# Performance work log

Hardware: AMD Instinct MI355X
Metric: run time of the kernel (lower is better)

## Reference

```python
import jax, jax.numpy as jnp
import numpy as np

D_MODEL = 512
N_HEADS = 8
D_HEAD = D_MODEL // N_HEADS
EPS = 1e-5


def layer_norm(x, g, b):
    mu = jnp.mean(x, axis=-1, keepdims=True)
    var = jnp.mean(jnp.square(x - mu), axis=-1, keepdims=True)
    return (x - mu) * jax.lax.rsqrt(var + EPS) * g + b


def setup_inputs() -> dict:
    key = jax.random.key(0)
    ks = jax.random.split(key, 8)
    B, L, D = 2, 4096, D_MODEL
    x = jax.random.normal(ks[0], (B, L, D), dtype=jnp.float32)
    # monotonically increasing event timestamps (hours)
    timestamps = jnp.sort(jax.random.uniform(ks[1], (B, L), dtype=jnp.float32) * 1000.0, axis=-1)
    mask = jnp.ones((B, L), dtype=jnp.float32)
    s = 0.02
    return {
        "x": x,
        "timestamps": timestamps,
        "mask": mask,
        "ln1_g": jnp.ones((D,), jnp.float32),
        "ln1_b": jnp.zeros((D,), jnp.float32),
        "w_qkv": jax.random.normal(ks[2], (3 * D, D), jnp.float32) * s,
        "w_out": jax.random.normal(ks[3], (D, D), jnp.float32) * s,
        "decay_rate": jnp.ones((N_HEADS,), jnp.float32) * 0.01,
        "ln2_g": jnp.ones((D,), jnp.float32),
        "ln2_b": jnp.zeros((D,), jnp.float32),
        "w_ff1": jax.random.normal(ks[4], (4 * D, D), jnp.float32) * s,
        "w_ff2": jax.random.normal(ks[5], (D, 4 * D), jnp.float32) * s,
    }


def reference(x, timestamps, mask, ln1_g, ln1_b, w_qkv, w_out, decay_rate, ln2_g, ln2_b, w_ff1, w_ff2):
    B, L, D = x.shape
    H, dh = N_HEADS, D_HEAD
    scale = dh ** (-0.5)

    xn = layer_norm(x, ln1_g, ln1_b)
    qkv = (xn @ w_qkv.T).reshape(B, L, 3, H, dh).transpose(2, 0, 3, 1, 4)  # [3,B,H,L,dh]
    q, k, v = qkv[0], qkv[1], qkv[2]

    attn = jnp.einsum("bhid,bhjd->bhij", q, k) * scale  # [B,H,L,L]

    # temporal-decay bias
    t_diff = jnp.abs(timestamps[:, None, :, None] - timestamps[:, None, None, :]) / 24.0  # [B,1,L,L]
    decay = jax.nn.softplus(decay_rate)[None, :, None, None]  # [1,H,1,1]
    attn = attn - decay * t_diff

    # causal mask
    causal = jnp.triu(jnp.ones((L, L), dtype=bool), k=1)
    attn = jnp.where(causal[None, None], -jnp.inf, attn)

    # padding mask over keys
    pad = (mask == 0)[:, None, None, :]  # [B,1,1,L]
    attn = jnp.where(pad, -jnp.inf, attn)

    attn = jax.nn.softmax(attn, axis=-1)
    out = jnp.einsum("bhij,bhjd->bhid", attn, v).transpose(0, 2, 1, 3).reshape(B, L, D)

    x = x + out @ w_out.T
    h = layer_norm(x, ln2_g, ln2_b)
    x = x + jax.nn.silu(h @ w_ff1.T) @ w_ff2.T
    return x
```

## Files before the change

### kernel.cpp

```cpp
#include <hip/hip_runtime.h>
#include <hip/hip_bf16.h>
#include <cmath>


#define L_SEQ 4096
#define D_MODEL 512
#define N_HEADS 8
#define D_HEAD 64
#define QKV_LD 1536

typedef __attribute__((ext_vector_type(8))) short bf16x8;
typedef __attribute__((ext_vector_type(4))) float f32x4;
typedef __attribute__((ext_vector_type(4))) unsigned u32x4;

__device__ __forceinline__ __hip_bfloat16 f2bf(float v) { return __float2bfloat16(v); }

__device__ __forceinline__ float exp2_raw(float x) {
  float r;
  asm("v_exp_f32 %0, %1" : "=v"(r) : "v"(x));
  return r;
}

__device__ __forceinline__ void gl_lds16(const __hip_bfloat16* g, __hip_bfloat16* l) {
  __builtin_amdgcn_global_load_lds((__attribute__((address_space(1))) void*)g,
                                   (__attribute__((address_space(3))) void*)l, 16, 0, 0);
}

__global__ __launch_bounds__(256) void cvt4b_kernel(const float* __restrict__ s0, __hip_bfloat16* __restrict__ d0,
                                                    const float* __restrict__ s1, __hip_bfloat16* __restrict__ d1,
                                                    const float* __restrict__ s2, __hip_bfloat16* __restrict__ d2,
                                                    const float* __restrict__ s3, __hip_bfloat16* __restrict__ d3,
                                                    const float* __restrict__ ts,
                                                    const float* __restrict__ mask,
                                                    const float* __restrict__ decay_rate,
                                                    float* __restrict__ biasH) {
  const int i = blockIdx.x * 256 + threadIdx.x;
  if (i < 786432) {
    const float* s;
    __hip_bfloat16* d;
    int off;
    if (i < 196608) { s = s0; d = d0; off = i; }
    else if (i < 262144) { s = s1; d = d1; off = i - 196608; }
    else if (i < 524288) { s = s2; d = d2; off = i - 262144; }
    else { s = s3; d = d3; off = i - 524288; }
    const float4 v = ((const float4*)s)[off];
    d[4 * off + 0] = f2bf(v.x);
    d[4 * off + 1] = f2bf(v.y);
    d[4 * off + 2] = f2bf(v.z);
    d[4 * off + 3] = f2bf(v.w);
  } else {
    const int idx = i - 786432;
    const int col = idx & 4095;
    const int h = (idx >> 12) & 7;
    const int b = idx >> 15;
    const float LOG2E = 1.4426950408889634f;
    const float dfac = log1pf(expf(decay_rate[h])) * (1.0f / 24.0f) * LOG2E;
    const float m = mask[b * 4096 + col];
    biasH[idx] = dfac * ts[b * 4096 + col] + (m != 0.f ? 0.f : -1e30f);
  }
}

__global__ __launch_bounds__(256) void ln_kernel(const float* __restrict__ x,
                                                 const float* __restrict__ g,
                                                 const float* __restrict__ b,
                                                 __hip_bfloat16* __restrict__ out) {
  const int row = blockIdx.x;
  const int t = threadIdx.x;
  const float* xr = x + (size_t)row * D_MODEL;
  float v0 = xr[t];
  float v1 = xr[t + 256];
  float s = v0 + v1;
  float qq = v0 * v0 + v1 * v1;
  for (int off = 32; off > 0; off >>= 1) {
    s += __shfl_xor(s, off);
    qq += __shfl_xor(qq, off);
  }
  __shared__ float red[8];
  const int wid = t >> 6;
  if ((t & 63) == 0) { red[wid] = s; red[4 + wid] = qq; }
  __syncthreads();
  s = red[0] + red[1] + red[2] + red[3];
  qq = red[4] + red[5] + red[6] + red[7];
  const float mu = s * (1.0f / 512.0f);
  const float var = fmaxf(qq * (1.0f / 512.0f) - mu * mu, 0.0f);
  const float rstd = rsqrtf(var + 1e-5f);
  __hip_bfloat16* orow = out + (size_t)row * D_MODEL;
  orow[t] = f2bf((v0 - mu) * rstd * g[t] + b[t]);
  orow[t + 256] = f2bf((v1 - mu) * rstd * g[t + 256] + b[t + 256]);
}

__global__ __launch_bounds__(256) void vtrans_kernel(const __hip_bfloat16* __restrict__ qkv,
                                                     __hip_bfloat16* __restrict__ vt) {
  const int gid = blockIdx.x * 256 + threadIdx.x;
  const int l = gid & 4095;
  const int bg = gid >> 12;
  const int b = bg >> 6, g = bg & 63;
  const int h = g >> 3, dg = (g & 7) * 8;
  const __hip_bfloat16* src = qkv + (size_t)(b * L_SEQ + l) * QKV_LD + 1024 + h * 64 + dg;
  bf16x8 v = *(const bf16x8*)src;
  const int kin = l & 63;
  const int sl = (kin & 0x23) | ((kin & 0x10) >> 2) | ((kin & 0x0c) << 1);
  const size_t dbase = (size_t)((b * 8 + h) * 64 + dg) * L_SEQ + (l & ~63) + sl;
  for (int j = 0; j < 8; j++)
    vt[dbase + (size_t)j * L_SEQ] = ((const __hip_bfloat16*)&v)[j];
}

template <int EPI>
__global__ __launch_bounds__(256) void gemm_kernel(const __hip_bfloat16* __restrict__ A,
                                                   const __hip_bfloat16* __restrict__ B,
                                                   int M, int N, int K,
                                                   const float* __restrict__ aux,
                                                   void* __restrict__ C) {
  __shared__ __align__(16) __hip_bfloat16 As[2][128 * 32];
  __shared__ __align__(16) __hip_bfloat16 Bs[2][128 * 32];
  const int tid = threadIdx.x;
  const int lane = tid & 63, w = tid >> 6;
  const int m0 = blockIdx.y * 128, n0 = blockIdx.x * 128;
  const int wm = (w >> 1) * 64, wn = (w & 1) * 64;
  const int r = lane & 15, q = lane >> 4;

  f32x4 acc[4][4];
  const f32x4 zz = {0.f, 0.f, 0.f, 0.f};
  for (int i = 0; i < 4; i++)
    for (int j = 0; j < 4; j++) acc[i][j] = zz;

  const int c0 = tid, c1 = 256 + tid;
  const int row0 = c0 >> 2, kb0 = (c0 & 3) * 8;
  const int row1 = c1 >> 2, kb1 = (c1 & 3) * 8;

#define GEMM_STAGE(k0, buf)                                                     \
  do {                                                                          \
    gl_lds16(A + (size_t)(m0 + row0) * K + ((k0) + kb0), &As[buf][c0 * 8]);     \
    gl_lds16(B + (size_t)(n0 + row0) * K + ((k0) + kb0), &Bs[buf][c0 * 8]);     \
    gl_lds16(A + (size_t)(m0 + row1) * K + ((k0) + kb1), &As[buf][c1 * 8]);     \
    gl_lds16(B + (size_t)(n0 + row1) * K + ((k0) + kb1), &Bs[buf][c1 * 8]);     \
  } while (0)

  GEMM_STAGE(0, 0);
  const int niter = K >> 5;
  for (int it = 0; it < niter; it++) {
    const int cur = it & 1;
    if (it + 1 < niter) {
      GEMM_STAGE((it + 1) << 5, cur ^ 1);
      asm volatile("s_waitcnt vmcnt(4)" ::: "memory");
    } else {
      asm volatile("s_waitcnt vmcnt(0)" ::: "memory");
    }
    __builtin_amdgcn_s_barrier();
    bf16x8 af[4], bfr[4];
    for (int mi = 0; mi < 4; mi++)
      af[mi] = *(const bf16x8*)(&As[cur][(wm + mi * 16 + r) * 32 + q * 8]);
    for (int ni = 0; ni < 4; ni++)
      bfr[ni] = *(const bf16x8*)(&Bs[cur][(wn + ni * 16 + r) * 32 + q * 8]);
    for (int mi = 0; mi < 4; mi++)
      for (int ni = 0; ni < 4; ni++)
        acc[mi][ni] = __builtin_amdgcn_mfma_f32_16x16x32_bf16(af[mi], bfr[ni], acc[mi][ni], 0, 0, 0);
    __builtin_amdgcn_s_barrier();
  }
#undef GEMM_STAGE

  for (int mi = 0; mi < 4; mi++)
    for (int ni = 0; ni < 4; ni++)
      for (int j = 0; j < 4; j++) {
        const int gm = m0 + wm + mi * 16 + q * 4 + j;
        const int gn = n0 + wn + ni * 16 + r;
        float v = acc[mi][ni][j];
        const size_t idx = (size_t)gm * N + gn;
        if (EPI == 0) {
          ((__hip_bfloat16*)C)[idx] = f2bf(v);
        } else {
          v = v / (1.0f + expf(-v));
          ((__hip_bfloat16*)C)[idx] = f2bf(v);
        }
      }
}

__global__ __launch_bounds__(256) void gemm_res64_kernel(const __hip_bfloat16* __restrict__ A,
                                                         const __hip_bfloat16* __restrict__ B,
                                                         int M, int N, int K,
                                                         const float* __restrict__ aux,
                                                         float* __restrict__ C) {
  __shared__ __align__(16) __hip_bfloat16 As[2][64 * 32];
  __shared__ __align__(16) __hip_bfloat16 Bs[2][128 * 32];
  const int tid = threadIdx.x;
  const int lane = tid & 63, w = tid >> 6;
  const int m0 = blockIdx.y * 64, n0 = blockIdx.x * 128;
  const int wm = (w >> 1) * 32, wn = (w & 1) * 64;
  const int r = lane & 15, q = lane >> 4;

  f32x4 acc[2][4];
  const f32x4 zz = {0.f, 0.f, 0.f, 0.f};
  for (int i = 0; i < 2; i++)
    for (int j = 0; j < 4; j++) acc[i][j] = zz;

  const int rowA = tid >> 2, kbA = (tid & 3) * 8;
  const int c0 = tid, c1 = 256 + tid;
  const int rowB0 = c0 >> 2, kb0 = (c0 & 3) * 8;
  const int rowB1 = c1 >> 2, kb1 = (c1 & 3) * 8;

#define GEMM_STAGE64(k0, buf)                                                    \
  do {                                                                           \
    gl_lds16(A + (size_t)(m0 + rowA) * K + ((k0) + kbA), &As[buf][tid * 8]);     \
    gl_lds16(B + (size_t)(n0 + rowB0) * K + ((k0) + kb0), &Bs[buf][c0 * 8]);     \
    gl_lds16(B + (size_t)(n0 + rowB1) * K + ((k0) + kb1), &Bs[buf][c1 * 8]);     \
  } while (0)

  GEMM_STAGE64(0, 0);
  const int niter = K >> 5;
  for (int it = 0; it < niter; it++) {
    const int cur = it & 1;
    if (it + 1 < niter) {
      GEMM_STAGE64((it + 1) << 5, cur ^ 1);
      asm volatile("s_waitcnt vmcnt(3)" ::: "memory");
    } else {
      asm volatile("s_waitcnt vmcnt(0)" ::: "memory");
    }
    __builtin_amdgcn_s_barrier();
    bf16x8 af[2], bfr[4];
    for (int mi = 0; mi < 2; mi++)
      af[mi] = *(const bf16x8*)(&As[cur][(wm + mi * 16 + r) * 32 + q * 8]);
    for (int ni = 0; ni < 4; ni++)
      bfr[ni] = *(const bf16x8*)(&Bs[cur][(wn + ni * 16 + r) * 32 + q * 8]);
    for (int mi = 0; mi < 2; mi++)
      for (int ni = 0; ni < 4; ni++)
        acc[mi][ni] = __builtin_amdgcn_mfma_f32_16x16x32_bf16(af[mi], bfr[ni], acc[mi][ni], 0, 0, 0);
    __builtin_amdgcn_s_barrier();
  }
#undef GEMM_STAGE64

  for (int mi = 0; mi < 2; mi++)
    for (int ni = 0; ni < 4; ni++)
      for (int j = 0; j < 4; j++) {
        const int gm = m0 + wm + mi * 16 + q * 4 + j;
        const int gn = n0 + wn + ni * 16 + r;
        const size_t idx = (size_t)gm * N + gn;
        C[idx] = acc[mi][ni][j] + aux[idx];
      }
}

__device__ __forceinline__ void stage_kv128_w2(int w, int lane, int key0,
                                               const __hip_bfloat16* __restrict__ Kg,
                                               const __hip_bfloat16* __restrict__ Vg,
                                               __hip_bfloat16* Ks, __hip_bfloat16* Vs) {
  const int krow_in = lane >> 3;
  const int kcs = (lane & 7) ^ krow_in;
  const int vrow_in = lane >> 4;
  const int vch = lane & 15;
#pragma unroll
  for (int ii = 0; ii < 8; ii++) {
    const int i = w * 8 + ii;
    const int krow = i * 8 + krow_in;
    gl_lds16(Kg + (size_t)(key0 + krow) * QKV_LD + kcs * 8, Ks + i * 512 + lane * 8);
    const int vrow = i * 4 + vrow_in;
    const int vcs = vch ^ (vrow & 7);
    gl_lds16(Vg + (size_t)vrow * L_SEQ + key0 + vcs * 8, Vs + i * 512 + lane * 8);
  }
}

template <bool CAUSAL>
__device__ __forceinline__ void attn_tile128d(int key0, int lw0a, int r, int q,
                                              const __hip_bfloat16* Ks,
                                              const __hip_bfloat16* Vs,
                                              const float* biasLds, float scale2,
                                              const bf16x8& qfa0, const bf16x8& qfa1,
                                              const bf16x8& qfb0, const bf16x8& qfb1,
                                              const bf16x8& onesf,
                                              f32x4* oa, f32x4* ob, f32x4& lsa, f32x4& lsb) {
  const int r7 = r & 7;
  const f32x4 zz = {0.f, 0.f, 0.f, 0.f};
  f32x4 bias4[8];
#pragma unroll
  for (int hc = 0; hc < 8; hc++)
    bias4[hc] = *(const f32x4*)(biasLds + key0 + hc * 16 + q * 4);
  f32x4 sa[8], sb[8];
  __builtin_amdgcn_s_setprio(1);
#pragma unroll
  for (int hc = 0; hc < 8; hc++) {
    const __hip_bfloat16* kr = Ks + (hc * 16 + r) * 64;
    bf16x8 k0 = *(const bf16x8*)(kr + ((q ^ r7) * 8));
    bf16x8 k1 = *(const bf16x8*)(kr + (((q + 4) ^ r7) * 8));
    f32x4 a = __builtin_amdgcn_mfma_f32_16x16x32_bf16(k0, qfa0, zz, 0, 0, 0);
    a = __builtin_amdgcn_mfma_f32_16x16x32_bf16(k1, qfa1, a, 0, 0, 0);
    sa[hc] = a;
    f32x4 bb = __builtin_amdgcn_mfma_f32_16x16x32_bf16(k0, qfb0, zz, 0, 0, 0);
    bb = __builtin_amdgcn_mfma_f32_16x16x32_bf16(k1, qfb1, bb, 0, 0, 0);
    sb[hc] = bb;
  }
  __builtin_amdgcn_s_setprio(0);
  float pa_[8][4], pb_[8][4];
#pragma unroll
  for (int hc = 0; hc < 8; hc++)
#pragma unroll
    for (int j = 0; j < 4; j++) {
      const int key = key0 + hc * 16 + q * 4 + j;
      float pva = exp2_raw(fmaf(sa[hc][j], scale2, bias4[hc][j]));
      float pvb = exp2_raw(fmaf(sb[hc][j], scale2, bias4[hc][j]));
      if (CAUSAL) {
        pva = (key <= lw0a + r) ? pva : 0.f;
        pvb = (key <= lw0a + 16 + r) ? pvb : 0.f;
      }
      pa_[hc][j] = pva;
      pb_[hc][j] = pvb;
    }
  bf16x8 paa[4], pab[4];
#pragma unroll
  for (int kc = 0; kc < 4; kc++) {
    u32x4 pw;
    unsigned w0, w1, w2, w3;
    asm("v_cvt_pk_bf16_f32 %0, %1, %2" : "=v"(w0) : "v"(pa_[2 * kc][0]), "v"(pa_[2 * kc][1]));
    asm("v_cvt_pk_bf16_f32 %0, %1, %2" : "=v"(w1) : "v"(pa_[2 * kc][2]), "v"(pa_[2 * kc][3]));
    asm("v_cvt_pk_bf16_f32 %0, %1, %2" : "=v"(w2) : "v"(pa_[2 * kc + 1][0]), "v"(pa_[2 * kc + 1][1]));
    asm("v_cvt_pk_bf16_f32 %0, %1, %2" : "=v"(w3) : "v"(pa_[2 * kc + 1][2]), "v"(pa_[2 * kc + 1][3]));
    pw[0] = w0; pw[1] = w1; pw[2] = w2; pw[3] = w3;
    paa[kc] = *(bf16x8*)&pw;
    asm("v_cvt_pk_bf16_f32 %0, %1, %2" : "=v"(w0) : "v"(pb_[2 * kc][0]), "v"(pb_[2 * kc][1]));
    asm("v_cvt_pk_bf16_f32 %0, %1, %2" : "=v"(w1) : "v"(pb_[2 * kc][2]), "v"(pb_[2 * kc][3]));
    asm("v_cvt_pk_bf16_f32 %0, %1, %2" : "=v"(w2) : "v"(pb_[2 * kc + 1][0]), "v"(pb_[2 * kc + 1][1]));
    asm("v_cvt_pk_bf16_f32 %0, %1, %2" : "=v"(w3) : "v"(pb_[2 * kc + 1][2]), "v"(pb_[2 * kc + 1][3]));
    pw[0] = w0; pw[1] = w1; pw[2] = w2; pw[3] = w3;
    pab[kc] = *(bf16x8*)&pw;
  }
  __builtin_amdgcn_s_setprio(1);
#pragma unroll
  for (int kc = 0; kc < 4; kc++) {
#pragma unroll
    for (int c = 0; c < 4; c++) {
      const __hip_bfloat16* vr = Vs + (c * 16 + r) * 128 + (((kc * 4 + q) ^ r7) * 8);
      bf16x8 vf = *(const bf16x8*)vr;
      oa[c] = __builtin_amdgcn_mfma_f32_16x16x32_bf16(paa[kc], vf, oa[c], 0, 0, 0);
      ob[c] = __builtin_amdgcn_mfma_f32_16x16x32_bf16(pab[kc], vf, ob[c], 0, 0, 0);
    }
    lsa = __builtin_amdgcn_mfma_f32_16x16x32_bf16(paa[kc], onesf, lsa, 0, 0, 0);
    lsb = __builtin_amdgcn_mfma_f32_16x16x32_bf16(pab[kc], onesf, lsb, 0, 0, 0);
  }
  __builtin_amdgcn_s_setprio(0);
}

__global__ __launch_bounds__(128, 1) void attn_kernel(const __hip_bfloat16* __restrict__ qkv,
                                                      const __hip_bfloat16* __restrict__ vt,
                                                      const float* __restrict__ biasH,
                                                      __hip_bfloat16* __restrict__ out) {
  const int blk = blockIdx.x;
  const int bh = blk & 15;
  const int j = blk >> 4;
  const int b = bh >> 3, h = bh & 7;
  const int tid = threadIdx.x, lane = tid & 63, w = tid >> 6;
  const int r = lane & 15, q = lane >> 4;

  const int qi1 = j, qi2 = 63 - j;
  const int nt1 = (qi1 >> 1) + 1, nt2 = (qi2 >> 1) + 1;
  const int lwa1 = qi1 * 64 + w * 32;
  const int lwa2 = qi2 * 64 + w * 32;

  __shared__ __align__(16) __hip_bfloat16 Ksm[2][128 * 64];
  __shared__ __align__(16) __hip_bfloat16 Vsm[2][64 * 128];
  __shared__ __align__(16) float biasLds[4096];

  const float LOG2E = 1.4426950408889634f;
  const float scale2 = 0.125f * LOG2E;

  const __hip_bfloat16* Kg = qkv + (size_t)b * L_SEQ * QKV_LD + 512 + h * 64;
  const __hip_bfloat16* Vg = vt + (size_t)bh * 64 * L_SEQ;
  const float* biasHp = biasH + (size_t)bh * L_SEQ;

  stage_kv128_w2(w, lane, 0, Kg, Vg, Ksm[0], Vsm[0]);
#pragma unroll
  for (int ii = 0; ii < 8; ii++) {
    const int fo = (w * 8 + ii) * 256;
    gl_lds16((const __hip_bfloat16*)(biasHp + fo + lane * 4),
             (__hip_bfloat16*)(biasLds + fo + lane * 4));
  }

  bf16x8 qfa0, qfa1, qfb0, qfb1;
  {
    const __hip_bfloat16* qa = qkv + (size_t)(b * L_SEQ + lwa1 + r) * QKV_LD + h * 64 + q * 8;
    qfa0 = *(const bf16x8*)qa;
    qfa1 = *(const bf16x8*)(qa + 32);
    const __hip_bfloat16* qb = qa + (size_t)16 * QKV_LD;
    qfb0 = *(const bf16x8*)qb;
    qfb1 = *(const bf16x8*)(qb + 32);
  }

  const f32x4 zz = {0.f, 0.f, 0.f, 0.f};
  f32x4 oa[4], ob[4];
  for (int c = 0; c < 4; c++) { oa[c] = zz; ob[c] = zz; }
  f32x4 lsa = zz, lsb = zz;

  bf16x8 onesf;
  for (int i = 0; i < 8; i++) ((short*)&onesf)[i] = (short)0x3F80;

  for (int t = 0; t < nt1; t++) {
    const int cur = t & 1;
    const int nk = (t + 1 < nt1) ? (t + 1) : 0;
    stage_kv128_w2(w, lane, nk << 7, Kg, Vg, Ksm[cur ^ 1], Vsm[cur ^ 1]);
    asm volatile("s_waitcnt vmcnt(16)" ::: "memory");
    __builtin_amdgcn_s_barrier();
    if (t == nt1 - 1)
      attn_tile128d<true>(t << 7, lwa1, r, q, Ksm[cur], Vsm[cur], biasLds, scale2,
                          qfa0, qfa1, qfb0, qfb1, onesf, oa, ob, lsa, lsb);
    else
      attn_tile128d<false>(t << 7, lwa1, r, q, Ksm[cur], Vsm[cur], biasLds, scale2,
                           qfa0, qfa1, qfb0, qfb1, onesf, oa, ob, lsa, lsb);
    __builtin_amdgcn_s_barrier();
  }

  {
    float ija[4], ijb[4];
    for (int jj = 0; jj < 4; jj++) { ija[jj] = 1.0f / lsa[jj]; ijb[jj] = 1.0f / lsb[jj]; }
    for (int c = 0; c < 4; c++)
      for (int jj = 0; jj < 4; jj++) {
        const int ra = lwa1 + q * 4 + jj;
        out[(size_t)(b * L_SEQ + ra) * D_MODEL + h * 64 + c * 16 + r] = f2bf(oa[c][jj] * ija[jj]);
        out[(size_t)(b * L_SEQ + ra + 16) * D_MODEL + h * 64 + c * 16 + r] = f2bf(ob[c][jj] * ijb[jj]);
      }
    for (int c = 0; c < 4; c++) { oa[c] = zz; ob[c] = zz; }
    lsa = zz; lsb = zz;
    const __hip_bfloat16* qa = qkv + (size_t)(b * L_SEQ + lwa2 + r) * QKV_LD + h * 64 + q * 8;
    qfa0 = *(const bf16x8*)qa;
    qfa1 = *(const bf16x8*)(qa + 32);
    const __hip_bfloat16* qb = qa + (size_t)16 * QKV_LD;
    qfb0 = *(const bf16x8*)qb;
    qfb1 = *(const bf16x8*)(qb + 32);
  }

  for (int t = 0; t < nt2; t++) {
    const int cur = (nt1 + t) & 1;
    if (t + 1 < nt2) {
      stage_kv128_w2(w, lane, (t + 1) << 7, Kg, Vg, Ksm[cur ^ 1], Vsm[cur ^ 1]);
      asm volatile("s_waitcnt vmcnt(16)" ::: "memory");
    } else {
      asm volatile("s_waitcnt vmcnt(0)" ::: "memory");
    }
    __builtin_amdgcn_s_barrier();
    if (t == nt2 - 1)
      attn_tile128d<true>(t << 7, lwa2, r, q, Ksm[cur], Vsm[cur], biasLds, scale2,
                          qfa0, qfa1, qfb0, qfb1, onesf, oa, ob, lsa, lsb);
    else
      attn_tile128d<false>(t << 7, lwa2, r, q, Ksm[cur], Vsm[cur], biasLds, scale2,
                           qfa0, qfa1, qfb0, qfb1, onesf, oa, ob, lsa, lsb);
    __builtin_amdgcn_s_barrier();
  }

  {
    float ija[4], ijb[4];
    for (int jj = 0; jj < 4; jj++) { ija[jj] = 1.0f / lsa[jj]; ijb[jj] = 1.0f / lsb[jj]; }
    for (int c = 0; c < 4; c++)
      for (int jj = 0; jj < 4; jj++) {
        const int ra = lwa2 + q * 4 + jj;
        out[(size_t)(b * L_SEQ + ra) * D_MODEL + h * 64 + c * 16 + r] = f2bf(oa[c][jj] * ija[jj]);
        out[(size_t)(b * L_SEQ + ra + 16) * D_MODEL + h * 64 + c * 16 + r] = f2bf(ob[c][jj] * ijb[jj]);
      }
  }
}

extern "C" void kernel_launch(void* const* d_in, const int* in_sizes, int n_in,
                              void* d_out, int out_size, void* d_ws, size_t ws_size,
                              hipStream_t stream) {
  const float* x = (const float*)d_in[0];
  const float* ts = (const float*)d_in[1];
  const float* mask = (const float*)d_in[2];
  const float* ln1_g = (const float*)d_in[3];
  const float* ln1_b = (const float*)d_in[4];
  const float* w_qkv = (const float*)d_in[5];
  const float* w_out = (const float*)d_in[6];
  const float* decay = (const float*)d_in[7];
  const float* ln2_g = (const float*)d_in[8];
  const float* ln2_b = (const float*)d_in[9];
  const float* w_ff1 = (const float*)d_in[10];
  const float* w_ff2 = (const float*)d_in[11];

  char* ws = (char*)d_ws;
  __hip_bfloat16* wqkv_b = (__hip_bfloat16*)(ws + 0);
  __hip_bfloat16* wout_b = (__hip_bfloat16*)(ws + 1572864);
  __hip_bfloat16* wff1_b = (__hip_bfloat16*)(ws + 2097152);
  __hip_bfloat16* wff2_b = (__hip_bfloat16*)(ws + 4194304);
  __hip_bfloat16* xn = (__hip_bfloat16*)(ws + 6291456);
  __hip_bfloat16* vt = (__hip_bfloat16*)(ws + 6291456);
  __hip_bfloat16* qkv = (__hip_bfloat16*)(ws + 14680064);
  __hip_bfloat16* attnout = (__hip_bfloat16*)(ws + 39845888);
  __hip_bfloat16* h = attnout;
  __hip_bfloat16* ff1out = (__hip_bfloat16*)(ws + 6291456);
  float* x2 = (float*)(ws + 48234496);
  float* biasH = (float*)(ws + 48234496);
  float* out = (float*)d_out;

  const int M = 2 * L_SEQ;

  cvt4b_kernel<<<dim3(3328), dim3(256), 0, stream>>>(w_qkv, wqkv_b, w_out, wout_b,
                                                     w_ff1, wff1_b, w_ff2, wff2_b,
                                                     ts, mask, decay, biasH);

  ln_kernel<<<dim3(M), dim3(256), 0, stream>>>(x, ln1_g, ln1_b, xn);
  gemm_kernel<0><<<dim3(12, 64), dim3(256), 0, stream>>>(xn, wqkv_b, M, 1536, 512, nullptr, qkv);
  vtrans_kernel<<<dim3(2048), dim3(256), 0, stream>>>(qkv, vt);
  attn_kernel<<<dim3(512), dim3(128), 0, stream>>>(qkv, vt, biasH, attnout);
  gemm_res64_kernel<<<dim3(4, 128), dim3(256), 0, stream>>>(attnout, wout_b, M, 512, 512, x, x2);
  ln_kernel<<<dim3(M), dim3(256), 0, stream>>>(x2, ln2_g, ln2_b, h);
  gemm_kernel<2><<<dim3(16, 64), dim3(256), 0, stream>>>(h, wff1_b, M, 2048, 512, nullptr, ff1out);
  gemm_res64_kernel<<<dim3(4, 128), dim3(256), 0, stream>>>(ff1out, wff2_b, M, 512, 2048, x2, out);
}
```

Before: 295.0 us.

## Process paired causal query tiles concurrently with four waves sharing KV stages

The attention kernel goes from 2 waves that handle the short and long causal query tiles one after the other to 4 waves: two handle the short tile and two the long tile at the same time. The K/V tiles staged in LDS are shared by both groups, so each key block is loaded once per block instead of once per query tile. The KV loading work is spread over 4 waves and the waitcnt thresholds are adjusted to match. In exchange, the short-tile waves sit idle at barriers once their tile is finished, and the larger block may lower occupancy.

New measurement: 283.0 us. 4.1% less time.

```diff
diff --git a/kernel.cpp b/kernel.cpp
--- a/kernel.cpp
+++ b/kernel.cpp
@@ -238,7 +238,7 @@
       }
 }
 
-__device__ __forceinline__ void stage_kv128_w2(int w, int lane, int key0,
+__device__ __forceinline__ void stage_kv128_w4(int w, int lane, int key0,
                                                const __hip_bfloat16* __restrict__ Kg,
                                                const __hip_bfloat16* __restrict__ Vg,
                                                __hip_bfloat16* Ks, __hip_bfloat16* Vs) {
@@ -247,8 +247,8 @@
   const int vrow_in = lane >> 4;
   const int vch = lane & 15;
 #pragma unroll
-  for (int ii = 0; ii < 8; ii++) {
-    const int i = w * 8 + ii;
+  for (int ii = 0; ii < 4; ii++) {
+    const int i = w * 4 + ii;
     const int krow = i * 8 + krow_in;
     gl_lds16(Kg + (size_t)(key0 + krow) * QKV_LD + kcs * 8, Ks + i * 512 + lane * 8);
     const int vrow = i * 4 + vrow_in;
@@ -336,21 +336,19 @@
   __builtin_amdgcn_s_setprio(0);
 }
 
-__global__ __launch_bounds__(128, 1) void attn_kernel(const __hip_bfloat16* __restrict__ qkv,
+__global__ __launch_bounds__(256, 2) void attn_kernel(const __hip_bfloat16* __restrict__ qkv,
                                                       const __hip_bfloat16* __restrict__ vt,
                                                       const float* __restrict__ biasH,
                                                       __hip_bfloat16* __restrict__ out) {
   const int blk = blockIdx.x;
   const int bh = blk & 15;
-  const int j = blk >> 4;
+  const int pr = blk >> 4;
   const int b = bh >> 3, h = bh & 7;
   const int tid = threadIdx.x, lane = tid & 63, w = tid >> 6;
+  const int grp = w >> 1, wsub = w & 1;
+  const int qi = grp ? (63 - pr) : pr;
+  const int lw0a = qi * 64 + wsub * 32;
   const int r = lane & 15, q = lane >> 4;
-
-  const int qi1 = j, qi2 = 63 - j;
-  const int nt1 = (qi1 >> 1) + 1, nt2 = (qi2 >> 1) + 1;
-  const int lwa1 = qi1 * 64 + w * 32;
-  const int lwa2 = qi2 * 64 + w * 32;
 
   __shared__ __align__(16) __hip_bfloat16 Ksm[2][128 * 64];
   __shared__ __align__(16) __hip_bfloat16 Vsm[2][64 * 128];
@@ -363,17 +361,17 @@
   const __hip_bfloat16* Vg = vt + (size_t)bh * 64 * L_SEQ;
   const float* biasHp = biasH + (size_t)bh * L_SEQ;
 
-  stage_kv128_w2(w, lane, 0, Kg, Vg, Ksm[0], Vsm[0]);
-#pragma unroll
-  for (int ii = 0; ii < 8; ii++) {
-    const int fo = (w * 8 + ii) * 256;
+  stage_kv128_w4(w, lane, 0, Kg, Vg, Ksm[0], Vsm[0]);
+#pragma unroll
+  for (int ii = 0; ii < 4; ii++) {
+    const int fo = (w * 4 + ii) * 256;
     gl_lds16((const __hip_bfloat16*)(biasHp + fo + lane * 4),
              (__hip_bfloat16*)(biasLds + fo + lane * 4));
   }
 
   bf16x8 qfa0, qfa1, qfb0, qfb1;
   {
-    const __hip_bfloat16* qa = qkv + (size_t)(b * L_SEQ + lwa1 + r) * QKV_LD + h * 64 + q * 8;
+    const __hip_bfloat16* qa = qkv + (size_t)(b * L_SEQ + lw0a + r) * QKV_LD + h * 64 + q * 8;
     qfa0 = *(const bf16x8*)qa;
     qfa1 = *(const bf16x8*)(qa + 32);
     const __hip_bfloat16* qb = qa + (size_t)16 * QKV_LD;
@@ -389,68 +387,38 @@
   bf16x8 onesf;
   for (int i = 0; i < 8; i++) ((short*)&onesf)[i] = (short)0x3F80;
 
-  for (int t = 0; t < nt1; t++) {
+  const int ntA = (pr >> 1) + 1;
+  const int ntB = ((63 - pr) >> 1) + 1;
+  const int nt = grp ? ntB : ntA;
+
+  for (int t = 0; t < ntB; t++) {
     const int cur = t & 1;
-    const int nk = (t + 1 < nt1) ? (t + 1) : 0;
-    stage_kv128_w2(w, lane, nk << 7, Kg, Vg, Ksm[cur ^ 1], Vsm[cur ^ 1]);
-    asm volatile("s_waitcnt vmcnt(16)" ::: "memory");
-    __builtin_amdgcn_s_barrier();
-    if (t == nt1 - 1)
-      attn_tile128d<true>(t << 7, lwa1, r, q, Ksm[cur], Vsm[cur], biasLds, scale2,
-                          qfa0, qfa1, qfb0, qfb1, onesf, oa, ob, lsa, lsb);
-    else
-      attn_tile128d<false>(t << 7, lwa1, r, q, Ksm[cur], Vsm[cur], biasLds, scale2,
-                           qfa0, qfa1, qfb0, qfb1, onesf, oa, ob, lsa, lsb);
-    __builtin_amdgcn_s_barrier();
-  }
-
-  {
-    float ija[4], ijb[4];
-    for (int jj = 0; jj < 4; jj++) { ija[jj] = 1.0f / lsa[jj]; ijb[jj] = 1.0f / lsb[jj]; }
-    for (int c = 0; c < 4; c++)
-      for (int jj = 0; jj < 4; jj++) {
-        const int ra = lwa1 + q * 4 + jj;
-        out[(size_t)(b * L_SEQ + ra) * D_MODEL + h * 64 + c * 16 + r] = f2bf(oa[c][jj] * ija[jj]);
-        out[(size_t)(b * L_SEQ + ra + 16) * D_MODEL + h * 64 + c * 16 + r] = f2bf(ob[c][jj] * ijb[jj]);
-      }
-    for (int c = 0; c < 4; c++) { oa[c] = zz; ob[c] = zz; }
-    lsa = zz; lsb = zz;
-    const __hip_bfloat16* qa = qkv + (size_t)(b * L_SEQ + lwa2 + r) * QKV_LD + h * 64 + q * 8;
-    qfa0 = *(const bf16x8*)qa;
-    qfa1 = *(const bf16x8*)(qa + 32);
-    const __hip_bfloat16* qb = qa + (size_t)16 * QKV_LD;
-    qfb0 = *(const bf16x8*)qb;
-    qfb1 = *(const bf16x8*)(qb + 32);
-  }
-
-  for (int t = 0; t < nt2; t++) {
-    const int cur = (nt1 + t) & 1;
-    if (t + 1 < nt2) {
-      stage_kv128_w2(w, lane, (t + 1) << 7, Kg, Vg, Ksm[cur ^ 1], Vsm[cur ^ 1]);
-      asm volatile("s_waitcnt vmcnt(16)" ::: "memory");
+    if (t + 1 < ntB) {
+      stage_kv128_w4(w, lane, (t + 1) << 7, Kg, Vg, Ksm[cur ^ 1], Vsm[cur ^ 1]);
+      asm volatile("s_waitcnt vmcnt(8)" ::: "memory");
     } else {
       asm volatile("s_waitcnt vmcnt(0)" ::: "memory");
     }
     __builtin_amdgcn_s_barrier();
-    if (t == nt2 - 1)
-      attn_tile128d<true>(t << 7, lwa2, r, q, Ksm[cur], Vsm[cur], biasLds, scale2,
-                          qfa0, qfa1, qfb0, qfb1, onesf, oa, ob, lsa, lsb);
-    else
-      attn_tile128d<false>(t << 7, lwa2, r, q, Ksm[cur], Vsm[cur], biasLds, scale2,
-                           qfa0, qfa1, qfb0, qfb1, onesf, oa, ob, lsa, lsb);
-    __builtin_amdgcn_s_barrier();
-  }
-
-  {
-    float ija[4], ijb[4];
-    for (int jj = 0; jj < 4; jj++) { ija[jj] = 1.0f / lsa[jj]; ijb[jj] = 1.0f / lsb[jj]; }
-    for (int c = 0; c < 4; c++)
-      for (int jj = 0; jj < 4; jj++) {
-        const int ra = lwa2 + q * 4 + jj;
-        out[(size_t)(b * L_SEQ + ra) * D_MODEL + h * 64 + c * 16 + r] = f2bf(oa[c][jj] * ija[jj]);
-        out[(size_t)(b * L_SEQ + ra + 16) * D_MODEL + h * 64 + c * 16 + r] = f2bf(ob[c][jj] * ijb[jj]);
-      }
-  }
+    if (t < nt) {
+      if (t == nt - 1)
+        attn_tile128d<true>(t << 7, lw0a, r, q, Ksm[cur], Vsm[cur], biasLds, scale2,
+                            qfa0, qfa1, qfb0, qfb1, onesf, oa, ob, lsa, lsb);
+      else
+        attn_tile128d<false>(t << 7, lw0a, r, q, Ksm[cur], Vsm[cur], biasLds, scale2,
+                             qfa0, qfa1, qfb0, qfb1, onesf, oa, ob, lsa, lsb);
+    }
+    __builtin_amdgcn_s_barrier();
+  }
+
+  float ija[4], ijb[4];
+  for (int jj = 0; jj < 4; jj++) { ija[jj] = 1.0f / lsa[jj]; ijb[jj] = 1.0f / lsb[jj]; }
+  for (int c = 0; c < 4; c++)
+    for (int jj = 0; jj < 4; jj++) {
+      const int ra = lw0a + q * 4 + jj;
+      out[(size_t)(b * L_SEQ + ra) * D_MODEL + h * 64 + c * 16 + r] = f2bf(oa[c][jj] * ija[jj]);
+      out[(size_t)(b * L_SEQ + ra + 16) * D_MODEL + h * 64 + c * 16 + r] = f2bf(ob[c][jj] * ijb[jj]);
+    }
 }
 
 extern "C" void kernel_launch(void* const* d_in, const int* in_sizes, int n_in,
@@ -493,7 +461,7 @@
   ln_kernel<<<dim3(M), dim3(256), 0, stream>>>(x, ln1_g, ln1_b, xn);
   gemm_kernel<0><<<dim3(12, 64), dim3(256), 0, stream>>>(xn, wqkv_b, M, 1536, 512, nullptr, qkv);
   vtrans_kernel<<<dim3(2048), dim3(256), 0, stream>>>(qkv, vt);
-  attn_kernel<<<dim3(512), dim3(128), 0, stream>>>(qkv, vt, biasH, attnout);
+  attn_kernel<<<dim3(512), dim3(256), 0, stream>>>(qkv, vt, biasH, attnout);
   gemm_res64_kernel<<<dim3(4, 128), dim3(256), 0, stream>>>(attnout, wout_b, M, 512, 512, x, x2);
   ln_kernel<<<dim3(M), dim3(256), 0, stream>>>(x2, ln2_g, ln2_b, h);
   gemm_kernel<2><<<dim3(16, 64), dim3(256), 0, stream>>>(h, wff1_b, M, 2048, 512, nullptr, ff1out);
```
